# Kernel optimization log

Hardware: AMD Instinct MI355X
Metric: run time of the kernel (lower is better)

The kernel has to match this reference:

```python
import jax, jax.numpy as jnp
import numpy as np

B, T, D, H = 2, 2048, 1024, 16


def setup_inputs() -> dict:
    key = jax.random.key(0)
    ks = jax.random.split(key, 5)
    s = 0.02  # small init so softmax is well-behaved
    return {
        "x": jax.random.normal(ks[0], (B, T, D), dtype=jnp.float32),
        "Wq": jax.random.normal(ks[1], (D, D), dtype=jnp.float32) * s,
        "bq": jnp.zeros((D,), dtype=jnp.float32),
        "Wk": jax.random.normal(ks[2], (D, D), dtype=jnp.float32) * s,
        "bk": jnp.zeros((D,), dtype=jnp.float32),
        "Wv": jax.random.normal(ks[3], (D, D), dtype=jnp.float32) * s,
        "bv": jnp.zeros((D,), dtype=jnp.float32),
        "Wo": jax.random.normal(ks[4], (D, D), dtype=jnp.float32) * s,
        "bo": jnp.zeros((D,), dtype=jnp.float32),
    }


def _split_heads(t):
    # (B,T,D) -> (B,H,T,d_k)
    b, tt, dd = t.shape
    return t.reshape(b, tt, H, dd // H).transpose(0, 2, 1, 3)


def reference(x, Wq, bq, Wk, bk, Wv, bv, Wo, bo):
    d_k = D // H
    q = _split_heads(x @ Wq + bq)  # (B,H,T,d_k)
    k = _split_heads(x @ Wk + bk)
    v = _split_heads(x @ Wv + bv)
    # scaled dot-product similarities: (B,H,T,T)
    scores = jnp.einsum("bhqd,bhkd->bhqk", q, k) / jnp.sqrt(jnp.asarray(d_k, dtype=x.dtype))
    causal = jnp.tril(jnp.ones((T, T), dtype=bool))  # True = keep
    scores = jnp.where(causal, scores, jnp.asarray(-jnp.inf, dtype=scores.dtype))
    probs = jax.nn.softmax(scores, axis=-1)
    attn = jnp.einsum("bhqk,bhkd->bhqd", probs, v)  # (B,H,T,d_k)
    merged = attn.transpose(0, 2, 1, 3).reshape(B, T, D)  # (B,T,D)
    return merged @ Wo + bo
```

## Files before the change

kernel.cpp:

```cpp
#include <hip/hip_runtime.h>
#include <hip/hip_bf16.h>
#include <cstdint>
#include <cstddef>

#define B_  2
#define T_  2048
#define D_  1024
#define H_  16
#define DK_ 64

typedef __hip_bfloat16 bf16;
typedef __bf16 bf16x8 __attribute__((ext_vector_type(8)));
typedef float  f32x4  __attribute__((ext_vector_type(4)));

#define MFMA16(a, b, c) __builtin_amdgcn_mfma_f32_16x16x32_bf16((a), (b), (c), 0, 0, 0)

#define SCALE_Q 0.1803368801111137f

#if defined(__has_builtin)
#if __has_builtin(__builtin_amdgcn_exp2f)
#define FEXP2(x) __builtin_amdgcn_exp2f(x)
#endif
#endif
#ifndef FEXP2
__device__ static inline float fexp2_asm(float x) {
  float r; asm("v_exp_f32 %0, %1" : "=v"(r) : "v"(x)); return r;
}
#define FEXP2(x) fexp2_asm(x)
#endif

__device__ static inline void gld_lds16(const void* g, void* l) {
  __builtin_amdgcn_global_load_lds((const __attribute__((address_space(1))) void*)g,
                                   (__attribute__((address_space(3))) void*)l, 16, 0, 0);
}

__device__ static inline ushort f2bu(float x) {
  union { bf16 h; ushort u; } c;
  c.h = __float2bfloat16(x);
  return c.u;
}

__device__ static inline uint32_t cvtpk_bf16(float lo, float hi) {
  uint32_t r;
  asm volatile("v_cvt_pk_bf16_f32 %0, %1, %2" : "=v"(r) : "v"(lo), "v"(hi));
  return r;
}

__global__ __launch_bounds__(256) void pack_all_kernel(const float* __restrict__ x,
                                                       const float* __restrict__ Wq,
                                                       const float* __restrict__ Wk,
                                                       const float* __restrict__ Wv,
                                                       const float* __restrict__ Wo,
                                                       bf16* __restrict__ xb,
                                                       bf16* __restrict__ Wt,
                                                       bf16* __restrict__ Wot) {
  __shared__ bf16 t[64][65];
  const int bid = blockIdx.x;
  const int tid = threadIdx.x;
  if (bid < 4096) {
    const int i = bid * 256 + tid;
    const float4 v = reinterpret_cast<const float4*>(x)[i];
    union { ushort4 u; bf16 h[4]; } c;
    c.h[0] = __float2bfloat16(v.x);
    c.h[1] = __float2bfloat16(v.y);
    c.h[2] = __float2bfloat16(v.z);
    c.h[3] = __float2bfloat16(v.w);
    reinterpret_cast<ushort4*>(xb)[i] = c.u;
    return;
  }
  const int wb  = bid - 4096;
  const int mat  = wb >> 8;
  const int tile = wb & 255;
  const int tr = tile >> 4, tc = tile & 15;
  const float* W = (mat == 0) ? Wq : (mat == 1) ? Wk : (mat == 2) ? Wv : Wo;
#pragma unroll
  for (int i = 0; i < 16; ++i) {
    const int idx = i * 256 + tid;
    const int r = idx >> 6, c = idx & 63;
    t[r][c] = __float2bfloat16(W[(size_t)(tr * 64 + r) * D_ + tc * 64 + c]);
  }
  __syncthreads();
  bf16* dst = (mat == 3) ? Wot : (Wt + (size_t)mat * D_ * D_);
#pragma unroll
  for (int i = 0; i < 16; ++i) {
    const int idx = i * 256 + tid;
    const int n = idx >> 6, k = idx & 63;
    dst[(size_t)(tc * 64 + n) * D_ + tr * 64 + k] = t[k][n];
  }
}

__global__ __launch_bounds__(256, 3) void gemm_qkv_kernel(
    const bf16* __restrict__ A, const bf16* __restrict__ Bt,
    const float* __restrict__ bias0, const float* __restrict__ bias1,
    const float* __restrict__ bias2,
    bf16* __restrict__ Qb, bf16* __restrict__ Kb, bf16* __restrict__ Vt) {
  __shared__ bf16 As[128 * 32];
  __shared__ bf16 Bs[128 * 32];
  const int tid  = threadIdx.x;
  const int lane = tid & 63, wid = tid >> 6;
  const int wr = wid >> 1, wc = wid & 1;
  const int l15 = lane & 15, lhi = lane >> 4;
  const int mbase = blockIdx.y * 128, nbase = blockIdx.x * 128;

  f32x4 acc[4][4] = {};

  const int r0  = tid >> 2;
  const int kc0 = (tid & 3) * 8;
  char* AsB = (char*)As;
  char* BsB = (char*)Bs;

  for (int kt = 0; kt < D_; kt += 32) {
    gld_lds16(A  + (size_t)(mbase + r0)      * D_ + kt + kc0, AsB + wid * 1024);
    gld_lds16(A  + (size_t)(mbase + 64 + r0) * D_ + kt + kc0, AsB + 4096 + wid * 1024);
    gld_lds16(Bt + (size_t)(nbase + r0)      * D_ + kt + kc0, BsB + wid * 1024);
    gld_lds16(Bt + (size_t)(nbase + 64 + r0) * D_ + kt + kc0, BsB + 4096 + wid * 1024);
    __syncthreads();

    bf16x8 af[4], bfv[4];
#pragma unroll
    for (int m = 0; m < 4; ++m)
      af[m] = *reinterpret_cast<const bf16x8*>(&As[(wr * 64 + m * 16 + l15) * 32 + lhi * 8]);
#pragma unroll
    for (int n = 0; n < 4; ++n)
      bfv[n] = *reinterpret_cast<const bf16x8*>(&Bs[(wc * 64 + n * 16 + l15) * 32 + lhi * 8]);
#pragma unroll
    for (int m = 0; m < 4; ++m)
#pragma unroll
      for (int n = 0; n < 4; ++n)
        acc[m][n] = MFMA16(af[m], bfv[n], acc[m][n]);
    __syncthreads();
  }

#pragma unroll
  for (int n = 0; n < 4; ++n) {
    const int col = nbase + wc * 64 + n * 16 + l15;
    const int seg  = col >> 10;
    const int ncol = col & 1023;
    const float* bias = (seg == 0) ? bias0 : (seg == 1) ? bias1 : bias2;
    const float bv_ = bias[ncol];
    const int h = ncol >> 6, dk = ncol & 63;
    if (seg == 2) {
#pragma unroll
      for (int m = 0; m < 4; ++m) {
        const int t0 = mbase + wr * 64 + m * 16 + lhi * 4;
        const int b = t0 >> 11, t = t0 & 2047;
        union { ushort u[4]; uint2 v; } pk;
#pragma unroll
        for (int j = 0; j < 4; ++j) pk.u[j] = f2bu(acc[m][n][j] + bv_);
        *reinterpret_cast<uint2*>(&Vt[((size_t)(b * H_ + h) * DK_ + dk) * T_ + t]) = pk.v;
      }
    } else {
#pragma unroll
      for (int m = 0; m < 4; ++m) {
#pragma unroll
        for (int j = 0; j < 4; ++j) {
          const int row = mbase + wr * 64 + m * 16 + lhi * 4 + j;
          const int b = row >> 11, t = row & 2047;
          const int bh = b * H_ + h;
          float outv = acc[m][n][j] + bv_;
          if (seg == 0) outv *= SCALE_Q;
          const bf16 hv = __float2bfloat16(outv);
          if (seg == 0) Qb[((size_t)bh * T_ + t) * DK_ + dk] = hv;
          else          Kb[((size_t)bh * T_ + t) * DK_ + dk] = hv;
        }
      }
    }
  }
}

__global__ __launch_bounds__(256, 2) void gemm_out_kernel(
    const bf16* __restrict__ A, const bf16* __restrict__ Bt,
    const float* __restrict__ bias, float* __restrict__ outp) {
  __shared__ __align__(16) bf16 As[128 * 64];
  __shared__ __align__(16) bf16 Bs[64 * 64];
  const int tid  = threadIdx.x;
  const int lane = tid & 63, wid = tid >> 6;
  const int wr = wid >> 1, wc = wid & 1;
  const int l15 = lane & 15, lhi = lane >> 4;
  const int mbase = blockIdx.y * 128, nbase = blockIdx.x * 64;

  f32x4 acc[4][2] = {};

  const bf16* sa0; const bf16* sa1; const bf16* sa2; const bf16* sa3;
  const bf16* sb0; const bf16* sb1;
  {
    const int iA0 = tid, iA1 = 256 + tid, iA2 = 512 + tid, iA3 = 768 + tid;
    sa0 = A + (size_t)(mbase + (iA0 >> 3)) * D_ + (((iA0 & 7) ^ ((iA0 >> 3) & 7)) * 8);
    sa1 = A + (size_t)(mbase + (iA1 >> 3)) * D_ + (((iA1 & 7) ^ ((iA1 >> 3) & 7)) * 8);
    sa2 = A + (size_t)(mbase + (iA2 >> 3)) * D_ + (((iA2 & 7) ^ ((iA2 >> 3) & 7)) * 8);
    sa3 = A + (size_t)(mbase + (iA3 >> 3)) * D_ + (((iA3 & 7) ^ ((iA3 >> 3) & 7)) * 8);
    sb0 = Bt + (size_t)(nbase + (iA0 >> 3)) * D_ + (((iA0 & 7) ^ ((iA0 >> 3) & 7)) * 8);
    sb1 = Bt + (size_t)(nbase + (iA1 >> 3)) * D_ + (((iA1 & 7) ^ ((iA1 >> 3) & 7)) * 8);
  }
  const int ub = wid * 1024;

  for (int kt = 0; kt < D_; kt += 64) {
    gld_lds16(sa0 + kt, (char*)As + ub);
    gld_lds16(sa1 + kt, (char*)As + 4096 + ub);
    gld_lds16(sa2 + kt, (char*)As + 8192 + ub);
    gld_lds16(sa3 + kt, (char*)As + 12288 + ub);
    gld_lds16(sb0 + kt, (char*)Bs + ub);
    gld_lds16(sb1 + kt, (char*)Bs + 4096 + ub);
    __syncthreads();

    const int rsw = l15 & 7;
    bf16x8 af[4][2], bfv[2][2];
#pragma unroll
    for (int m = 0; m < 4; ++m)
#pragma unroll
      for (int kk = 0; kk < 2; ++kk)
        af[m][kk] = *reinterpret_cast<const bf16x8*>(
            (const char*)As + (wr * 64 + m * 16 + l15) * 128 + (((kk * 4 + lhi) ^ rsw) * 16));
#pragma unroll
    for (int n = 0; n < 2; ++n)
#pragma unroll
      for (int kk = 0; kk < 2; ++kk)
        bfv[n][kk] = *reinterpret_cast<const bf16x8*>(
            (const char*)Bs + (wc * 32 + n * 16 + l15) * 128 + (((kk * 4 + lhi) ^ rsw) * 16));
#pragma unroll
    for (int m = 0; m < 4; ++m)
#pragma unroll
      for (int n = 0; n < 2; ++n)
#pragma unroll
        for (int kk = 0; kk < 2; ++kk)
          acc[m][n] = MFMA16(af[m][kk], bfv[n][kk], acc[m][n]);
    __syncthreads();
  }

#pragma unroll
  for (int n = 0; n < 2; ++n) {
    const int col = nbase + wc * 32 + n * 16 + l15;
    const float bv_ = bias[col];
#pragma unroll
    for (int m = 0; m < 4; ++m)
#pragma unroll
      for (int j = 0; j < 4; ++j) {
        const int row = mbase + wr * 64 + m * 16 + lhi * 4 + j;
        outp[(size_t)row * D_ + col] = acc[m][n][j] + bv_;
      }
  }
}

__global__ __launch_bounds__(512, 4) void attn_kernel(const bf16* __restrict__ Q,
                                                      const bf16* __restrict__ Kg,
                                                      const bf16* __restrict__ Vt,
                                                      bf16* __restrict__ Mg) {
  __shared__ __align__(16) bf16 Kl[2][128 * 64];
  __shared__ __align__(16) bf16 Vl[2][64 * 128];
  const int tid = threadIdx.x, lane = tid & 63, wid = tid >> 6;
  const int l15 = lane & 15, lhi = lane >> 4;
  const int p  = blockIdx.x & 15;
  const int bh = blockIdx.x >> 4;
  const int half = wid >> 2, w4 = wid & 3;
  const int qtile = half ? (31 - p) : p;
  const int qbase = qtile * 64 + w4 * 16;
  const int b = bh >> 4, h = bh & 15;

  const bf16* Qp = Q  + (size_t)bh * T_ * DK_;
  const bf16* Kp = Kg + (size_t)bh * T_ * DK_;
  const bf16* Vp = Vt + (size_t)bh * DK_ * T_;

  const bf16x8 qf0 = *reinterpret_cast<const bf16x8*>(&Qp[(size_t)(qbase + l15) * DK_ + lhi * 8]);
  const bf16x8 qf1 = *reinterpret_cast<const bf16x8*>(&Qp[(size_t)(qbase + l15) * DK_ + 32 + lhi * 8]);

  bf16x8 onesb;
#pragma unroll
  for (int i = 0; i < 8; ++i) onesb[i] = (__bf16)1.0f;

  f32x4 o[4] = {};
  f32x4 lacc = {};
  float mrow = -1e30f;

  const int ntr = (33 - p) >> 1;

  const int iA = tid, iB = 512 + tid;
  const bf16* ks0 = Kp + (size_t)(iA >> 3) * DK_ + (((iA & 7) ^ ((iA >> 3) & 7)) * 8);
  const bf16* ks1 = Kp + (size_t)(iB >> 3) * DK_ + (((iB & 7) ^ ((iB >> 3) & 7)) * 8);
  const bf16* vs0 = Vp + (size_t)(iA >> 4) * T_ + (((iA & 15) ^ ((iA >> 4) & 15)) * 8);
  const bf16* vs1 = Vp + (size_t)(iB >> 4) * T_ + (((iB & 15) ^ ((iB >> 4) & 15)) * 8);
  const int ub0 = wid * 1024;
  const int ub1 = 8192 + wid * 1024;

  gld_lds16(ks0, (char*)Kl[0] + ub0);
  gld_lds16(ks1, (char*)Kl[0] + ub1);
  gld_lds16(vs0, (char*)Vl[0] + ub0);
  gld_lds16(vs1, (char*)Vl[0] + ub1);
  ks0 += 128 * DK_; ks1 += 128 * DK_; vs0 += 128; vs1 += 128;
  __syncthreads();

  for (int rnd = 0; rnd < ntr; ++rnd) {
    const int cur = rnd & 1;
    const char* Kb_ = cur ? (const char*)Kl[1] : (const char*)Kl[0];
    const char* Vb_ = cur ? (const char*)Vl[1] : (const char*)Vl[0];
    if (rnd + 1 < ntr) {
      char* Kn = cur ? (char*)Kl[0] : (char*)Kl[1];
      char* Vn = cur ? (char*)Vl[0] : (char*)Vl[1];
      gld_lds16(ks0, Kn + ub0);
      gld_lds16(ks1, Kn + ub1);
      gld_lds16(vs0, Vn + ub0);
      gld_lds16(vs1, Vn + ub1);
      ks0 += 128 * DK_; ks1 += 128 * DK_; vs0 += 128; vs1 += 128;
    }

#pragma unroll
    for (int sub = 0; sub < 2; ++sub) {
      const int kv0 = rnd * 128 + sub * 64;
      if (kv0 <= qbase + 15) {
        f32x4 sv[4];
        __builtin_amdgcn_s_setprio(1);
#pragma unroll
        for (int s = 0; s < 4; ++s) {
          const int cbase = kv0 + s * 16;
          if (cbase <= qbase + 15) {
            const int row = sub * 64 + s * 16 + l15;
            const int rsw = l15 & 7;
            const bf16x8 k0 = *reinterpret_cast<const bf16x8*>(Kb_ + row * 128 + ((lhi       ^ rsw) * 16));
            const bf16x8 k1 = *reinterpret_cast<const bf16x8*>(Kb_ + row * 128 + (((4 + lhi) ^ rsw) * 16));
            f32x4 z = {};
            z = MFMA16(k0, qf0, z);
            sv[s] = MFMA16(k1, qf1, z);
          } else {
#pragma unroll
            for (int j = 0; j < 4; ++j) sv[s][j] = -1e30f;
          }
        }
        __builtin_amdgcn_s_setprio(0);

#pragma unroll
        for (int s = 0; s < 4; ++s) {
          const int cbase = kv0 + s * 16;
          if (cbase <= qbase + 15 && cbase + 15 > qbase) {
            const int r = qbase + l15;
#pragma unroll
            for (int j = 0; j < 4; ++j) {
              const int c = cbase + lhi * 4 + j;
              sv[s][j] = (c <= r) ? sv[s][j] : -1e30f;
            }
          }
        }

        float ml = sv[0][0];
#pragma unroll
        for (int s = 0; s < 4; ++s)
#pragma unroll
          for (int j = 0; j < 4; ++j) ml = fmaxf(ml, sv[s][j]);

        if (__any(ml > mrow + 8.0f)) {
          float mx = ml;
          mx = fmaxf(mx, __shfl_xor(mx, 16, 64));
          mx = fmaxf(mx, __shfl_xor(mx, 32, 64));
          const float mn = fmaxf(mrow, mx);
          const float sc = FEXP2(mrow - mn);
          mrow = mn;
          const int sci = __float_as_int(sc);
#pragma unroll
          for (int j = 0; j < 4; ++j) {
            const float scj = __int_as_float(
                __builtin_amdgcn_ds_bpermute((lhi * 4 + j) * 4, sci));
            lacc[j] *= scj;
            o[0][j] *= scj; o[1][j] *= scj; o[2][j] *= scj; o[3][j] *= scj;
          }
        }
#pragma unroll
        for (int s = 0; s < 4; ++s)
#pragma unroll
          for (int j = 0; j < 4; ++j) sv[s][j] = FEXP2(sv[s][j] - mrow);

        const bool oddl = (lhi & 1) != 0;
        bf16x8 pf[2];
#pragma unroll
        for (int hh = 0; hh < 2; ++hh) {
          const uint32_t u0l = cvtpk_bf16(sv[2 * hh][0], sv[2 * hh][1]);
          const uint32_t u0h = cvtpk_bf16(sv[2 * hh][2], sv[2 * hh][3]);
          const uint32_t u1l = cvtpk_bf16(sv[2 * hh + 1][0], sv[2 * hh + 1][1]);
          const uint32_t u1h = cvtpk_bf16(sv[2 * hh + 1][2], sv[2 * hh + 1][3]);
          const uint32_t sl = oddl ? u0l : u1l;
          const uint32_t sh = oddl ? u0h : u1h;
          const uint32_t rl = (uint32_t)__shfl_xor((int)sl, 16, 64);
          const uint32_t rh = (uint32_t)__shfl_xor((int)sh, 16, 64);
          union { uint32_t w[4]; bf16x8 v; } fr;
          fr.w[0] = oddl ? rl : u0l;
          fr.w[1] = oddl ? rh : u0h;
          fr.w[2] = oddl ? u1l : rl;
          fr.w[3] = oddl ? u1h : rh;
          pf[hh] = fr.v;
        }

        const int pl = ((lhi & 1) << 1) | (lhi >> 1);
        bf16x8 vf[8];
#pragma unroll
        for (int d = 0; d < 4; ++d) {
          const int rowv = d * 16 + l15;
#pragma unroll
          for (int s2 = 0; s2 < 2; ++s2) {
            const int cread = sub * 8 + s2 * 4 + pl;
            vf[d * 2 + s2] = *reinterpret_cast<const bf16x8*>(
                Vb_ + rowv * 256 + ((cread ^ l15) * 16));
          }
        }

        __builtin_amdgcn_s_setprio(1);
#pragma unroll
        for (int d = 0; d < 4; ++d) {
          o[d] = MFMA16(pf[0], vf[d * 2 + 0], o[d]);
          o[d] = MFMA16(pf[1], vf[d * 2 + 1], o[d]);
        }
        lacc = MFMA16(pf[0], onesb, lacc);
        lacc = MFMA16(pf[1], onesb, lacc);
        __builtin_amdgcn_s_setprio(0);
      }
    }

    __syncthreads();
  }

#pragma unroll
  for (int j = 0; j < 4; ++j) {
    const float inv = 1.0f / lacc[j];
    const int tq = qbase + lhi * 4 + j;
#pragma unroll
    for (int d = 0; d < 4; ++d)
      Mg[((size_t)b * T_ + tq) * D_ + h * DK_ + d * 16 + l15] = __float2bfloat16(o[d][j] * inv);
  }
}

extern "C" void kernel_launch(void* const* d_in, const int* in_sizes, int n_in,
                              void* d_out, int out_size, void* d_ws, size_t ws_size,
                              hipStream_t stream) {
  (void)in_sizes; (void)n_in; (void)out_size; (void)ws_size;
  const float* x  = (const float*)d_in[0];
  const float* Wq = (const float*)d_in[1];
  const float* bq = (const float*)d_in[2];
  const float* Wk = (const float*)d_in[3];
  const float* bk = (const float*)d_in[4];
  const float* Wv = (const float*)d_in[5];
  const float* bv = (const float*)d_in[6];
  const float* Wo = (const float*)d_in[7];
  const float* bo = (const float*)d_in[8];
  float* out = (float*)d_out;

  char* ws = (char*)d_ws;
  bf16* xb  = (bf16*)(ws);
  bf16* Mg  = (bf16*)(ws);
  bf16* Wt  = (bf16*)(ws + (size_t)( 8u << 20));
  bf16* Wot = (bf16*)(ws + (size_t)(14u << 20));
  bf16* Qb  = (bf16*)(ws + (size_t)(16u << 20));
  bf16* Kb  = (bf16*)(ws + (size_t)(24u << 20));
  bf16* Vt  = (bf16*)(ws + (size_t)(32u << 20));

  pack_all_kernel<<<5120, 256, 0, stream>>>(x, Wq, Wk, Wv, Wo, xb, Wt, Wot);
  gemm_qkv_kernel<<<dim3(24, 32), 256, 0, stream>>>(xb, Wt, bq, bk, bv, Qb, Kb, Vt);
  attn_kernel<<<dim3(512), 512, 0, stream>>>(Qb, Kb, Vt, Mg);
  gemm_out_kernel<<<dim3(16, 32), 256, 0, stream>>>(Mg, Wot, bo, out);
}
```

Before: 104.5 us.

## Double QKV GEMM K-tile to 64 with XOR-swizzled LDS, hoist V loads

The QKV projection GEMM now stages a K-depth of 64 per iteration instead of 32, which halves the number of barrier pairs. The LDS layout is XOR-swizzled by row so that the MFMA fragment reads avoid bank conflicts. In the attention kernel, the V fragment LDS loads move ahead of the masking and softmax code so their latency overlaps that arithmetic. In exchange, the GEMM uses more LDS and more registers, which may lower occupancy below the launch-bound target of 3 blocks.

```diff
diff --git a/kernel.cpp b/kernel.cpp
--- a/kernel.cpp
+++ b/kernel.cpp
@@ -94,8 +94,8 @@
     const float* __restrict__ bias0, const float* __restrict__ bias1,
     const float* __restrict__ bias2,
     bf16* __restrict__ Qb, bf16* __restrict__ Kb, bf16* __restrict__ Vt) {
-  __shared__ bf16 As[128 * 32];
-  __shared__ bf16 Bs[128 * 32];
+  __shared__ __align__(16) bf16 As[128 * 64];
+  __shared__ __align__(16) bf16 Bs[128 * 64];
   const int tid  = threadIdx.x;
   const int lane = tid & 63, wid = tid >> 6;
   const int wr = wid >> 1, wc = wid & 1;
@@ -104,30 +104,45 @@
 
   f32x4 acc[4][4] = {};
 
-  const int r0  = tid >> 2;
-  const int kc0 = (tid & 3) * 8;
-  char* AsB = (char*)As;
-  char* BsB = (char*)Bs;
-
-  for (int kt = 0; kt < D_; kt += 32) {
-    gld_lds16(A  + (size_t)(mbase + r0)      * D_ + kt + kc0, AsB + wid * 1024);
-    gld_lds16(A  + (size_t)(mbase + 64 + r0) * D_ + kt + kc0, AsB + 4096 + wid * 1024);
-    gld_lds16(Bt + (size_t)(nbase + r0)      * D_ + kt + kc0, BsB + wid * 1024);
-    gld_lds16(Bt + (size_t)(nbase + 64 + r0) * D_ + kt + kc0, BsB + 4096 + wid * 1024);
+  const bf16* sa[4]; const bf16* sb[4];
+#pragma unroll
+  for (int it = 0; it < 4; ++it) {
+    const int idx = it * 256 + tid;
+    const int r = idx >> 3, cs = ((idx & 7) ^ ((idx >> 3) & 7)) * 8;
+    sa[it] = A  + (size_t)(mbase + r) * D_ + cs;
+    sb[it] = Bt + (size_t)(nbase + r) * D_ + cs;
+  }
+  const int ub = wid * 1024;
+
+  for (int kt = 0; kt < D_; kt += 64) {
+#pragma unroll
+    for (int it = 0; it < 4; ++it) {
+      gld_lds16(sa[it] + kt, (char*)As + it * 4096 + ub);
+      gld_lds16(sb[it] + kt, (char*)Bs + it * 4096 + ub);
+    }
     __syncthreads();
 
-    bf16x8 af[4], bfv[4];
+    const int rsw = l15 & 7;
+    bf16x8 af[4][2], bfv[4][2];
 #pragma unroll
     for (int m = 0; m < 4; ++m)
-      af[m] = *reinterpret_cast<const bf16x8*>(&As[(wr * 64 + m * 16 + l15) * 32 + lhi * 8]);
+#pragma unroll
+      for (int kk = 0; kk < 2; ++kk)
+        af[m][kk] = *reinterpret_cast<const bf16x8*>(
+            (const char*)As + (wr * 64 + m * 16 + l15) * 128 + (((kk * 4 + lhi) ^ rsw) * 16));
 #pragma unroll
     for (int n = 0; n < 4; ++n)
-      bfv[n] = *reinterpret_cast<const bf16x8*>(&Bs[(wc * 64 + n * 16 + l15) * 32 + lhi * 8]);
+#pragma unroll
+      for (int kk = 0; kk < 2; ++kk)
+        bfv[n][kk] = *reinterpret_cast<const bf16x8*>(
+            (const char*)Bs + (wc * 64 + n * 16 + l15) * 128 + (((kk * 4 + lhi) ^ rsw) * 16));
 #pragma unroll
     for (int m = 0; m < 4; ++m)
 #pragma unroll
       for (int n = 0; n < 4; ++n)
-        acc[m][n] = MFMA16(af[m], bfv[n], acc[m][n]);
+#pragma unroll
+        for (int kk = 0; kk < 2; ++kk)
+          acc[m][n] = MFMA16(af[m][kk], bfv[n][kk], acc[m][n]);
     __syncthreads();
   }
 
@@ -325,6 +340,19 @@
           }
         }
         __builtin_amdgcn_s_setprio(0);
+
+        const int pl = ((lhi & 1) << 1) | (lhi >> 1);
+        bf16x8 vf[8];
+#pragma unroll
+        for (int d = 0; d < 4; ++d) {
+          const int rowv = d * 16 + l15;
+#pragma unroll
+          for (int s2 = 0; s2 < 2; ++s2) {
+            const int cread = sub * 8 + s2 * 4 + pl;
+            vf[d * 2 + s2] = *reinterpret_cast<const bf16x8*>(
+                Vb_ + rowv * 256 + ((cread ^ l15) * 16));
+          }
+        }
 
 #pragma unroll
         for (int s = 0; s < 4; ++s) {
@@ -386,19 +414,6 @@
           pf[hh] = fr.v;
         }
 
-        const int pl = ((lhi & 1) << 1) | (lhi >> 1);
-        bf16x8 vf[8];
-#pragma unroll
-        for (int d = 0; d < 4; ++d) {
-          const int rowv = d * 16 + l15;
-#pragma unroll
-          for (int s2 = 0; s2 < 2; ++s2) {
-            const int cread = sub * 8 + s2 * 4 + pl;
-            vf[d * 2 + s2] = *reinterpret_cast<const bf16x8*>(
-                Vb_ + rowv * 256 + ((cread ^ l15) * 16));
-          }
-        }
-
         __builtin_amdgcn_s_setprio(1);
 #pragma unroll
         for (int d = 0; d < 4; ++d) {
```

Measured after the change: 98.49 us. 5.7% less time.
